# Kernel optimization log

Measured on AMD Instinct MI355X. Metric: run time of the kernel, lower is better.

## Reference

```python
import jax, jax.numpy as jnp
import numpy as np


def _sobel_filters():
    # fil is the 3x3 smoothing kernel [[1,2,1],[2,4,2],[1,2,1]]
    fil = np.array([[1, 2, 1], [2, 4, 2], [1, 2, 1]], dtype=np.float32)
    fx = np.zeros((3, 3, 3), dtype=np.float32)
    fx[0, :, :] = fil
    fx[2, :, :] = -fil
    fy = np.zeros((3, 3, 3), dtype=np.float32)
    fy[:, 0, :] = fil
    fy[:, 2, :] = -fil
    fz = np.zeros((3, 3, 3), dtype=np.float32)
    fz[:, :, 0] = fil
    fz[:, :, 2] = -fil
    # Stack the three fixed (non-learned) filters as 3 output channels: [O=3, I=1, 3,3,3]
    return jnp.asarray(np.stack([fx, fy, fz])[:, None])


_FILT = _sobel_filters()
_DN = ('NCDHW', 'OIDHW', 'NCDHW')


def _grad3d(v):
    # v: [N,1,D,H,W] -> [N,3,D,H,W], padding=1 == SAME for 3x3x3 stride 1
    return jax.lax.conv_general_dilated(
        v, _FILT.astype(v.dtype), window_strides=(1, 1, 1),
        padding='SAME', dimension_numbers=_DN)


def setup_inputs() -> dict:
    key = jax.random.key(0)
    k1, k2 = jax.random.split(key)
    shape = (2, 1, 160, 192, 224)
    x = jax.random.normal(k1, shape, dtype=jnp.float32)
    y = jax.random.normal(k2, shape, dtype=jnp.float32)
    return {"x": x, "y": y}


def reference(x, y):
    gx = _grad3d(x)  # [N,3,D,H,W]
    gy = _grad3d(y)
    d2 = (gx - gy) ** 2
    # sum over the 3 directions of the per-direction MSE
    return jnp.sum(jnp.mean(d2, axis=(0, 2, 3, 4)))
```

## Files before the change

### kernel.cpp

```cpp
#include <hip/hip_runtime.h>
#include <stdint.h>


#define N_  2
#define D_  160
#define H_  192
#define W_  224
#define PS  (H_ * W_)

#define TD  16
#define TH  8
constexpr int SROWS = TH + 2;
constexpr int ROWF  = 224;
constexpr float SCALE = 1.0f / ((float)N_ * D_ * H_ * W_);

#define DMA16(gp, lp) __builtin_amdgcn_global_load_lds(                        \
    (const __attribute__((address_space(1))) void*)(gp),                       \
    (__attribute__((address_space(3))) void*)(lp), 16, 0, 0)

__global__ __launch_bounds__(256, 3)
void grad_loss_kernel(const float* __restrict__ x, const float* __restrict__ y,
                      float* __restrict__ out) {
    __shared__ float sbuf[3][SROWS][2][ROWF];
    __shared__ float wsum[4];

    const int tid  = threadIdx.x;
    const int lane = tid & 63;
    const int wv   = tid >> 6;

    const int h0 = blockIdx.y * TH;
    const int nchunks = D_ / TD;
    const int nb = blockIdx.z / nchunks;
    const int d0 = (blockIdx.z % nchunks) * TD;

    const float* vbx = x + (size_t)nb * ((size_t)D_ * PS);
    const float* vby = y + (size_t)nb * ((size_t)D_ * PS);

    int sl[5], sa[5], srw[5];
    const float* sb[5];
    #pragma unroll
    for (int k = 0; k < 5; ++k) {
        int item = 5 * wv + k;
        sl[k] = item >> 1;
        sa[k] = item & 1;
        int ghc = min(max(h0 - 1 + sl[k], 0), H_ - 1);
        srw[k] = ghc * W_;
        sb[k]  = sa[k] ? vby : vbx;
    }
    const int lo4 = lane * 4;

    auto stage = [&](int p, int bsel) {
        int pc = min(max(p, 0), D_ - 1);
        size_t poff = (size_t)pc * PS;
        if (lane < 56) {
            #pragma unroll
            for (int k = 0; k < 5; ++k)
                DMA16(sb[k] + poff + srw[k] + lo4, &sbuf[bsel][sl[k]][sa[k]][0]);
        }
    };

    const bool wact = lane < 56;
    float rmask[4];
    #pragma unroll
    for (int r = 0; r < 4; ++r) {
        int gh = h0 - 1 + 2 * wv + r;
        rmask[r] = (((unsigned)gh < (unsigned)H_) && wact) ? 1.f : 0.f;
    }
    const int lrd = (lane < 56 ? lane : 55) * 4;

    float4 A0[2], A1[2], A2[2], B0[2], B1[2], B2[2];
    const float4 z4 = make_float4(0.f, 0.f, 0.f, 0.f);
    #pragma unroll
    for (int j = 0; j < 2; ++j) { A0[j]=A1[j]=A2[j]=B0[j]=B1[j]=B2[j]=z4; }
    float acc = 0.f;

    stage(d0 - 1, 0);
    stage(d0,     1);

    for (int it = 0; it < TD + 2; ++it) {
        asm volatile("s_waitcnt vmcnt(5)\n\ts_barrier" ::: "memory");

        stage(d0 + 1 + it, (it + 2) % 3);

        const int q = d0 - 1 + it;
        const float pm = (q >= 0 && q < D_) ? 1.f : 0.f;
        const int bsel = it % 3;

        float4 sw[4], gw[4];
        #pragma unroll
        for (int r = 0; r < 4; ++r) {
            const int l = 2 * wv + r;
            const float4 xr = *(const float4*)&sbuf[bsel][l][0][lrd];
            const float4 yr = *(const float4*)&sbuf[bsel][l][1][lrd];
            const float m = rmask[r] * pm;
            float4 v = make_float4((xr.x - yr.x) * m, (xr.y - yr.y) * m,
                                   (xr.z - yr.z) * m, (xr.w - yr.w) * m);
            float Lm = __shfl_up(v.w, 1, 64);
            float Rp = __shfl_down(v.x, 1, 64);
            if (lane == 0) Lm = 0.f;
            sw[r] = make_float4(Lm + 2.f * v.x + v.y,
                                v.x + 2.f * v.y + v.z,
                                v.y + 2.f * v.z + v.w,
                                v.z + 2.f * v.w + Rp);
            gw[r] = make_float4(Lm - v.y, v.x - v.z, v.y - v.w, v.z - Rp);
        }
        float4 n0[2], n1[2], n2[2];
        #pragma unroll
        for (int j = 0; j < 2; ++j) {
            n0[j] = make_float4(sw[j].x + 2.f * sw[j+1].x + sw[j+2].x,
                                sw[j].y + 2.f * sw[j+1].y + sw[j+2].y,
                                sw[j].z + 2.f * sw[j+1].z + sw[j+2].z,
                                sw[j].w + 2.f * sw[j+1].w + sw[j+2].w);
            n1[j] = make_float4(sw[j].x - sw[j+2].x, sw[j].y - sw[j+2].y,
                                sw[j].z - sw[j+2].z, sw[j].w - sw[j+2].w);
            n2[j] = make_float4(gw[j].x + 2.f * gw[j+1].x + gw[j+2].x,
                                gw[j].y + 2.f * gw[j+1].y + gw[j+2].y,
                                gw[j].z + 2.f * gw[j+1].z + gw[j+2].z,
                                gw[j].w + 2.f * gw[j+1].w + gw[j+2].w);
        }

        if (it >= 2 && wact) {
            #pragma unroll
            for (int j = 0; j < 2; ++j) {
                float4 gx = make_float4(A0[j].x - n0[j].x, A0[j].y - n0[j].y,
                                        A0[j].z - n0[j].z, A0[j].w - n0[j].w);
                float4 gy = make_float4(A1[j].x + 2.f * B1[j].x + n1[j].x,
                                        A1[j].y + 2.f * B1[j].y + n1[j].y,
                                        A1[j].z + 2.f * B1[j].z + n1[j].z,
                                        A1[j].w + 2.f * B1[j].w + n1[j].w);
                float4 gz = make_float4(A2[j].x + 2.f * B2[j].x + n2[j].x,
                                        A2[j].y + 2.f * B2[j].y + n2[j].y,
                                        A2[j].z + 2.f * B2[j].z + n2[j].z,
                                        A2[j].w + 2.f * B2[j].w + n2[j].w);
                acc = fmaf(gx.x, gx.x, acc); acc = fmaf(gx.y, gx.y, acc);
                acc = fmaf(gx.z, gx.z, acc); acc = fmaf(gx.w, gx.w, acc);
                acc = fmaf(gy.x, gy.x, acc); acc = fmaf(gy.y, gy.y, acc);
                acc = fmaf(gy.z, gy.z, acc); acc = fmaf(gy.w, gy.w, acc);
                acc = fmaf(gz.x, gz.x, acc); acc = fmaf(gz.y, gz.y, acc);
                acc = fmaf(gz.z, gz.z, acc); acc = fmaf(gz.w, gz.w, acc);
            }
        }

        #pragma unroll
        for (int j = 0; j < 2; ++j) {
            A0[j] = B0[j]; A1[j] = B1[j]; A2[j] = B2[j];
            B0[j] = n0[j]; B1[j] = n1[j]; B2[j] = n2[j];
        }
    }

    asm volatile("s_waitcnt vmcnt(0)" ::: "memory");

    #pragma unroll
    for (int off = 32; off > 0; off >>= 1)
        acc += __shfl_xor(acc, off, 64);
    if (lane == 0) wsum[wv] = acc;
    __syncthreads();
    if (tid == 0) {
        float s = (wsum[0] + wsum[1]) + (wsum[2] + wsum[3]);
        atomicAdd(out, s * SCALE);
    }
}

extern "C" void kernel_launch(void* const* d_in, const int* in_sizes, int n_in,
                              void* d_out, int out_size, void* d_ws, size_t ws_size,
                              hipStream_t stream) {
    const float* x = (const float*)d_in[0];
    const float* y = (const float*)d_in[1];
    float* out = (float*)d_out;

    hipMemsetAsync(out, 0, sizeof(float), stream);

    dim3 block(256);
    dim3 grid(1,
              H_ / TH,
              N_ * (D_ / TD));
    grad_loss_kernel<<<grid, block, 0, stream>>>(x, y, out);
}
```

Measured before the change: 138.8 us.

## Replace direct-to-LDS DMA triple buffering with register-staged double buffering

Global loads now go into registers and are written to shared memory one iteration later, instead of going straight into LDS through global_load_lds. This cuts the buffer ring from three planes to two. The smaller LDS footprint lets launch bounds rise to 4 blocks per CU, aiming for more waves to hide memory latency. In exchange, prefetch distance shrinks from two planes to one, 20 extra VGPRs hold staged data, and each iteration pays for an extra LDS write pass.

```diff
diff --git a/kernel.cpp b/kernel.cpp
--- a/kernel.cpp
+++ b/kernel.cpp
@@ -14,14 +14,10 @@
 constexpr int ROWF  = 224;
 constexpr float SCALE = 1.0f / ((float)N_ * D_ * H_ * W_);
 
-#define DMA16(gp, lp) __builtin_amdgcn_global_load_lds(                        \
-    (const __attribute__((address_space(1))) void*)(gp),                       \
-    (__attribute__((address_space(3))) void*)(lp), 16, 0, 0)
-
-__global__ __launch_bounds__(256, 3)
+__global__ __launch_bounds__(256, 4)
 void grad_loss_kernel(const float* __restrict__ x, const float* __restrict__ y,
                       float* __restrict__ out) {
-    __shared__ float sbuf[3][SROWS][2][ROWF];
+    __shared__ float sbuf[2][SROWS][2][ROWF];
     __shared__ float wsum[4];
 
     const int tid  = threadIdx.x;
@@ -48,14 +44,24 @@
         sb[k]  = sa[k] ? vby : vbx;
     }
     const int lo4 = lane * 4;
+    const bool sact = lane < 56;
 
-    auto stage = [&](int p, int bsel) {
+    float4 rg[5];
+
+    auto rload = [&](int p) {
         int pc = min(max(p, 0), D_ - 1);
         size_t poff = (size_t)pc * PS;
-        if (lane < 56) {
+        if (sact) {
             #pragma unroll
             for (int k = 0; k < 5; ++k)
-                DMA16(sb[k] + poff + srw[k] + lo4, &sbuf[bsel][sl[k]][sa[k]][0]);
+                rg[k] = *(const float4*)(sb[k] + poff + srw[k] + lo4);
+        }
+    };
+    auto swrite = [&](int bsel) {
+        if (sact) {
+            #pragma unroll
+            for (int k = 0; k < 5; ++k)
+                *(float4*)&sbuf[bsel][sl[k]][sa[k]][lo4] = rg[k];
         }
     };
 
@@ -74,17 +80,19 @@
     for (int j = 0; j < 2; ++j) { A0[j]=A1[j]=A2[j]=B0[j]=B1[j]=B2[j]=z4; }
     float acc = 0.f;
 
-    stage(d0 - 1, 0);
-    stage(d0,     1);
+    rload(d0 - 1);
+    swrite(0);
+    rload(d0);
 
     for (int it = 0; it < TD + 2; ++it) {
-        asm volatile("s_waitcnt vmcnt(5)\n\ts_barrier" ::: "memory");
+        __syncthreads();
 
-        stage(d0 + 1 + it, (it + 2) % 3);
+        swrite((it + 1) & 1);
+        rload(d0 + 1 + it);
 
         const int q = d0 - 1 + it;
         const float pm = (q >= 0 && q < D_) ? 1.f : 0.f;
-        const int bsel = it % 3;
+        const int bsel = it & 1;
 
         float4 sw[4], gw[4];
         #pragma unroll
@@ -148,8 +156,6 @@
         }
     }
 
-    asm volatile("s_waitcnt vmcnt(0)" ::: "memory");
-
     #pragma unroll
     for (int off = 32; off > 0; off >>= 1)
         acc += __shfl_xor(acc, off, 64);
```

Measured after the change: 241.7 us. 1.74x slower.
